# Performance work log

Hardware: AMD Instinct MI355X
Metric: run time of the kernel (lower is better)

Reference implementation:

```python
import jax, jax.numpy as jnp
import numpy as np

N_NODES = 50000
N_EDGES = 800000
NEG_SLOPE = 0.2  # PyG GATv2Conv default
EPS = 1e-16      # PyG softmax denominator epsilon


def _segment_softmax(logits, seg, num_segments):
    # logits: [E, H]; seg: [E] target-node ids
    m = jax.ops.segment_max(logits, seg, num_segments=num_segments)
    p = jnp.exp(logits - m[seg])
    s = jax.ops.segment_sum(p, seg, num_segments=num_segments)
    return p / (s[seg] + EPS)


def _gatv2_conv(x, src, dst, Wl, Wr, att, bias, heads, out_ch, concat):
    # x: [N, F]; Wl/Wr: [F, heads*out_ch]; att: [heads, out_ch]
    n = x.shape[0]
    xl = (x @ Wl).reshape(n, heads, out_ch)
    xr = (x @ Wr).reshape(n, heads, out_ch)
    # GATv2: e_ij = att . leaky_relu(xl[j] + xr[i]) for edge j->i
    e = jax.nn.leaky_relu(xl[src] + xr[dst], NEG_SLOPE)  # [E, H, C]
    logit = jnp.einsum('ehc,hc->eh', e, att)             # [E, H]
    alpha = _segment_softmax(logit, dst, n)              # [E, H]
    out = jax.ops.segment_sum(alpha[:, :, None] * xl[src], dst, num_segments=n)  # [N, H, C]
    if concat:
        out = out.reshape(n, heads * out_ch)
    else:
        out = out.mean(axis=1)
    return out + bias


def setup_inputs() -> dict:
    key = jax.random.key(0)
    ks = jax.random.split(key, 20)
    in_ch, hid, out_ch, heads, edge_dim = 128, 128, 64, 8, 6
    c1 = hid // heads  # 16
    g = lambda k, shp, fan: (jax.random.normal(k, shp, jnp.float32) / np.sqrt(fan)).astype(jnp.float32)
    inp = {
        'x': jax.random.normal(ks[0], (N_NODES, in_ch), jnp.float32),
        'edge_index': jax.random.randint(ks[1], (2, N_EDGES), 0, N_NODES, dtype=jnp.int64),
        'edge_attr': jax.random.normal(ks[2], (N_EDGES, edge_dim), jnp.float32),
        'Wl1': g(ks[3], (in_ch, heads * c1), in_ch),
        'Wr1': g(ks[4], (in_ch, heads * c1), in_ch),
        'att1': g(ks[5], (heads, c1), c1),
        'b1': jnp.zeros((heads * c1,), jnp.float32),
        # layer 2: GATv2Conv(hid -> out_ch, heads=1, no concat)
        'Wl2': g(ks[6], (hid, out_ch), hid),
        'Wr2': g(ks[7], (hid, out_ch), hid),
        'att2': g(ks[8], (1, out_ch), out_ch),
        'b2': jnp.zeros((out_ch,), jnp.float32),
        # edge encoder (computed but unused downstream, as in the source)
        'We1': g(ks[9], (edge_dim, hid), edge_dim), 'be1': jnp.zeros((hid,), jnp.float32),
        'We2': g(ks[10], (hid, hid), hid), 'be2': jnp.zeros((hid,), jnp.float32),
        # classifier
        'Wc1': g(ks[11], (out_ch, hid), out_ch), 'bc1': jnp.zeros((hid,), jnp.float32),
        'Wc2': g(ks[12], (hid, 2), hid), 'bc2': jnp.zeros((2,), jnp.float32),
    }
    return inp


def reference(x, edge_index, edge_attr, Wl1, Wr1, att1, b1, Wl2, Wr2, att2, b2,
              We1, be1, We2, be2, Wc1, bc1, Wc2, bc2):
    n = x.shape[0]
    # edge encoder (dead code in the original forward; kept for fidelity)
    _edge_feats = jax.nn.relu(edge_attr @ We1 + be1) @ We2 + be2
    # add self-loops (PyG GATv2Conv default add_self_loops=True)
    loop = jnp.arange(n, dtype=edge_index.dtype)
    src = jnp.concatenate([edge_index[0], loop])
    dst = jnp.concatenate([edge_index[1], loop])
    # layer 1 (heads=8, concat) + relu; dropout is identity in eval
    h = _gatv2_conv(x, src, dst, Wl1, Wr1, att1, b1, heads=8, out_ch=16, concat=True)
    h = jax.nn.relu(h)
    # layer 2 (heads=1, mean)
    emb = _gatv2_conv(h, src, dst, Wl2, Wr2, att2, b2, heads=1, out_ch=64, concat=False)
    logits = jax.nn.relu(emb @ Wc1 + bc1) @ Wc2 + bc2
    return emb, logits
```

## Files before the change

kernel.cpp:

```cpp
#include <hip/hip_runtime.h>
#include <hip/hip_bf16.h>
#include <cfloat>

#define N_NODES 50000
#define N_EDGES 800000
#define E_TOT   850000
#define NEG_SLOPE 0.2f
#define SM_EPS 1e-16f
#define SCAN_B 196
#define LOG2E 1.4426950408889634f

#define NCH 32
#define CSZ 25000
#define NR  8
#define RSZ 6250

typedef __attribute__((ext_vector_type(8))) short short8;
typedef __attribute__((ext_vector_type(4))) float f32x4;

__device__ __forceinline__ float lrelu(float v) { return v > 0.0f ? v : NEG_SLOPE * v; }

__device__ __forceinline__ unsigned f2bf_pack2(float a, float b) {
    unsigned ua = __float_as_uint(a);
    ua += 0x7fff + ((ua >> 16) & 1);
    unsigned ub = __float_as_uint(b);
    ub += 0x7fff + ((ub >> 16) & 1);
    return (ua >> 16) | (ub & 0xffff0000u);
}
__device__ __forceinline__ unsigned short f2bf(float a) {
    unsigned ua = __float_as_uint(a);
    ua += 0x7fff + ((ua >> 16) & 1);
    return (unsigned short)(ua >> 16);
}
__device__ __forceinline__ float bf_lo(unsigned u) { return __uint_as_float(u << 16); }
__device__ __forceinline__ float bf_hi(unsigned u) { return __uint_as_float(u & 0xffff0000u); }

__device__ __forceinline__ unsigned short pack_one(const float* __restrict__ B0,
                                                   const float* __restrict__ B1,
                                                   int i, int N) {
    int m   = i / (128 * N);
    int rem = i % (128 * N);
    int j    = rem & 7;
    int quad = (rem >> 3) & 3;
    int n    = (rem >> 5) & 15;
    int ctk  = rem >> 9;
    int ct   = ctk % (N / 16);
    int kt   = ctk / (N / 16);
    int k    = kt * 32 + quad * 8 + j;
    int col  = ct * 16 + n;
    const float* B = m ? B1 : B0;
    return f2bf(B[k * N + col]);
}

__global__ void prep(const float* __restrict__ Wl1, const float* __restrict__ Wr1,
                     const float* __restrict__ Wl2, const float* __restrict__ Wr2,
                     const float* __restrict__ Wc1,
                     unsigned short* __restrict__ Bp1, unsigned short* __restrict__ Bp2,
                     unsigned short* __restrict__ Wc1p,
                     int* __restrict__ flags) {
    int i = blockIdx.x * 256 + threadIdx.x;
    if (i < 32768) {
        Bp1[i] = pack_one(Wl1, Wr1, i, 128);
    } else if (i < 49152) {
        Bp2[i - 32768] = pack_one(Wl2, Wr2, i - 32768, 64);
    } else if (i < 57344) {
        int idx = i - 49152;
        int j    = idx & 7;
        int quad = (idx >> 3) & 3;
        int n    = (idx >> 5) & 15;
        int ctk  = idx >> 9;
        int ct   = ctk & 7;
        int kt   = ctk >> 3;
        Wc1p[idx] = f2bf(Wc1[(kt * 32 + quad * 8 + j) * 128 + ct * 16 + n]);
    } else if (i < 57600) {
        flags[i - 57344] = 0;
    }
}

__device__ __forceinline__ void gemm128_both(int b, const float* __restrict__ x,
                                             const unsigned short* __restrict__ Bp1,
                                             unsigned short* __restrict__ xlbf,
                                             float* __restrict__ xr1, int M) {
    int w = threadIdx.x >> 6, lane = threadIdx.x & 63;
    int quad = lane >> 4, l16 = lane & 15;
    int row0 = b * 32 + (w & 1) * 16;
    int cb   = (w >> 1) * 64;
    f32x4 accL[4], accR[4];
    #pragma unroll
    for (int t = 0; t < 4; ++t) {
        accL[t] = (f32x4){0.f, 0.f, 0.f, 0.f};
        accR[t] = (f32x4){0.f, 0.f, 0.f, 0.f};
    }
    int arow = row0 + l16;
    bool aok = arow < M;
    #pragma unroll
    for (int kt = 0; kt < 4; ++kt) {
        short8 a = (short8)0;
        if (aok) {
            const float* Ap = x + (size_t)arow * 128 + quad * 8 + kt * 32;
            float4 f0 = *(const float4*)(Ap);
            float4 f1 = *(const float4*)(Ap + 4);
            union { uint4 u; short8 s; } cv;
            cv.u.x = f2bf_pack2(f0.x, f0.y);
            cv.u.y = f2bf_pack2(f0.z, f0.w);
            cv.u.z = f2bf_pack2(f1.x, f1.y);
            cv.u.w = f2bf_pack2(f1.z, f1.w);
            a = cv.s;
        }
        #pragma unroll
        for (int t = 0; t < 4; ++t) {
            int ct = (cb >> 4) + t;
            const short* bp = (const short*)Bp1 + (((kt * 8 + ct) * 16 + l16) * 4 + quad) * 8;
            short8 bL = *(const short8*)bp;
            short8 bR = *(const short8*)(bp + 128 * 128);
            accL[t] = __builtin_amdgcn_mfma_f32_16x16x32_bf16(a, bL, accL[t], 0, 0, 0);
            accR[t] = __builtin_amdgcn_mfma_f32_16x16x32_bf16(a, bR, accR[t], 0, 0, 0);
        }
    }
    #pragma unroll
    for (int t = 0; t < 4; ++t) {
        int col = cb + t * 16 + l16;
        #pragma unroll
        for (int r = 0; r < 4; ++r) {
            int row = row0 + quad * 4 + r;
            if (row < M) {
                xlbf[(size_t)row * 128 + col] = f2bf(accL[t][r]);
                xr1[(size_t)row * 128 + col]  = accR[t][r];
            }
        }
    }
}

__global__ __launch_bounds__(256)
void k2_count_gemms(const int* __restrict__ ei, unsigned* __restrict__ hist,
                    unsigned short* __restrict__ rank16,
                    const float* __restrict__ x, const unsigned short* __restrict__ Bp1,
                    unsigned short* __restrict__ xlbf, float* __restrict__ xr1, int M) {
    __shared__ unsigned hcnt[RSZ];
    int b = blockIdx.x;
    if (b < NR * NCH) {
        int r = b >> 5, c = b & 31;
        for (int i = threadIdx.x; i < RSZ; i += 256) hcnt[i] = 0;
        int nz = __syncthreads_or(ei[2 * threadIdx.x + 1]);
        int nlo = r * RSZ, nhi = nlo + RSZ;
        int cbeg = c * CSZ, cend = cbeg + CSZ;
        for (int e = cbeg + (int)threadIdx.x; e < cend; e += 1024) {
            int dd[4];
            #pragma unroll
            for (int j = 0; j < 4; ++j) {
                int ee = e + j * 256;
                dd[j] = -1;
                if (ee < cend)
                    dd[j] = nz ? ei[N_EDGES + ee] : ei[2 * N_EDGES + 2 * ee];
            }
            #pragma unroll
            for (int j = 0; j < 4; ++j) {
                int d = dd[j];
                if (d >= nlo && d < nhi) {
                    unsigned rk = atomicAdd(&hcnt[d - nlo], 1u);
                    rank16[e + j * 256] = (unsigned short)rk;
                }
            }
        }
        __syncthreads();
        unsigned* hp = hist + (size_t)(r * NCH + c) * RSZ;
        for (int i = threadIdx.x; i < RSZ; i += 256) hp[i] = hcnt[i];
    } else {
        gemm128_both(b - NR * NCH, x, Bp1, xlbf, xr1, M);
    }
}

__global__ void scan_fused(const unsigned* __restrict__ hist, int* __restrict__ rowptr,
                           int* __restrict__ esrc, int* __restrict__ bsum,
                           int* __restrict__ flags, int* __restrict__ base) {
    __shared__ int sh[256];
    int b = blockIdx.x, t = threadIdx.x, i = b * 256 + t;
    unsigned d[NCH];
    int tot = 0;
    int rr = 0, q = 0;
    if (i < N_NODES) {
        rr = i / RSZ; q = i - rr * RSZ;
        const unsigned* hp = hist + (size_t)rr * NCH * RSZ + q;
        #pragma unroll
        for (int c = 0; c < NCH; ++c) { d[c] = hp[(size_t)c * RSZ]; tot += (int)d[c]; }
    }
    int v = (i < N_NODES) ? tot + 1 : 0;
    sh[t] = v;
    __syncthreads();
    int val = v;
    for (int off = 1; off < 256; off <<= 1) {
        int add = (t >= off) ? sh[t - off] : 0;
        __syncthreads();
        val += add; sh[t] = val;
        __syncthreads();
    }
    if (t == 255) {
        bsum[b] = val;
        __threadfence();
        atomicExch(&flags[b], 1);
    }
    int contrib = 0;
    if (t < b) {
        while (atomicAdd(&flags[t], 0) == 0) {}
        contrib = atomicAdd(&bsum[t], 0);
    }
    __syncthreads();
    sh[t] = contrib;
    __syncthreads();
    #pragma unroll
    for (int off = 128; off; off >>= 1) {
        if (t < off) sh[t] += sh[t + off];
        __syncthreads();
    }
    int offset = sh[0];
    if (i < N_NODES) {
        int rp = (val - v) + offset;
        rowptr[i] = rp;
        esrc[rp] = i;
        int acc = rp + 1;
        int* bp = base + (size_t)rr * NCH * RSZ + q;
        #pragma unroll
        for (int c = 0; c < NCH; ++c) { bp[(size_t)c * RSZ] = acc; acc += (int)d[c]; }
    }
    if (i == 0) rowptr[N_NODES] = E_TOT;
}

__global__ void scatter_edges(const int* __restrict__ ei, const int* __restrict__ base,
                              const unsigned short* __restrict__ rank16,
                              int* __restrict__ esrc) {
    int nz = __syncthreads_or(ei[2 * threadIdx.x + 1]);
    int i = blockIdx.x * blockDim.x + threadIdx.x;
    if (2 * i >= N_EDGES) return;
    bool has2 = (2 * i + 1 < N_EDGES);
    int s0, d0, s1 = 0, d1 = 0;
    if (nz) {
        int2 sp = *(const int2*)(ei + 2 * i);
        int2 dp = *(const int2*)(ei + N_EDGES + 2 * i);
        s0 = sp.x; s1 = sp.y; d0 = dp.x; d1 = dp.y;
    } else {
        int4 sp = *(const int4*)(ei + 4 * i);
        int4 dp = *(const int4*)(ei + 2 * N_EDGES + 4 * i);
        s0 = sp.x; s1 = sp.z; d0 = dp.x; d1 = dp.z;
    }
    unsigned rr = *(const unsigned*)(rank16 + 2 * i);
    int e0 = 2 * i, e1 = 2 * i + 1;
    int c0 = e0 / CSZ, c1 = e1 / CSZ;
    int r0 = d0 / RSZ, r1 = d1 / RSZ;
    esrc[base[((size_t)r0 * NCH + c0) * RSZ + (d0 - r0 * RSZ)] + (int)(rr & 0xffffu)] = s0;
    if (has2)
        esrc[base[((size_t)r1 * NCH + c1) * RSZ + (d1 - r1 * RSZ)] + (int)(rr >> 16)] = s1;
}

__global__ __launch_bounds__(256)
void gemm_mfma64(const unsigned short* __restrict__ Abf, const unsigned short* __restrict__ Bp,
                 unsigned short* __restrict__ C0bf, float* __restrict__ C1, int M) {
    int w = threadIdx.x >> 6, lane = threadIdx.x & 63;
    int quad = lane >> 4, l16 = lane & 15;
    int matrix = w >> 1;
    int row0 = blockIdx.x * 32 + (w & 1) * 16;
    const unsigned short* Bm = Bp + matrix * 128 * 64;
    f32x4 acc[4];
    #pragma unroll
    for (int t = 0; t < 4; ++t) acc[t] = (f32x4){0.f, 0.f, 0.f, 0.f};
    int arow = row0 + l16;
    bool aok = arow < M;
    const short* Ap = (const short*)Abf + (size_t)arow * 128 + quad * 8;
    #pragma unroll
    for (int kt = 0; kt < 4; ++kt) {
        short8 a = (short8)0;
        if (aok) a = *(const short8*)(Ap + kt * 32);
        #pragma unroll
        for (int t = 0; t < 4; ++t) {
            const short* bp = (const short*)Bm + (((kt * 4 + t) * 16 + l16) * 4 + quad) * 8;
            short8 bfr = *(const short8*)bp;
            acc[t] = __builtin_amdgcn_mfma_f32_16x16x32_bf16(a, bfr, acc[t], 0, 0, 0);
        }
    }
    #pragma unroll
    for (int t = 0; t < 4; ++t) {
        int col = t * 16 + l16;
        #pragma unroll
        for (int r = 0; r < 4; ++r) {
            int row = row0 + quad * 4 + r;
            if (row < M) {
                if (matrix) C1[(size_t)row * 64 + col] = acc[t][r];
                else        C0bf[(size_t)row * 64 + col] = f2bf(acc[t][r]);
            }
        }
    }
}

__global__ __launch_bounds__(256)
void node_fused1(const int* __restrict__ rowptr, const int* __restrict__ esrc,
                 const unsigned short* __restrict__ xlbf, const float* __restrict__ xr,
                 const float* __restrict__ att, const float* __restrict__ b1,
                 unsigned short* __restrict__ hbf) {
    int wave = threadIdx.x >> 6;
    int lane = threadIdx.x & 63;
    int n = blockIdx.x * 4 + wave;
    int slot = lane >> 4;
    int l = lane & 15;
    int beg = rowptr[n], end = rowptr[n + 1];
    const float* xrp = xr + (size_t)n * 128 + 8 * l;
    float4 xra = *(const float4*)(xrp);
    float4 xrb = *(const float4*)(xrp + 4);
    float4 ata = *(const float4*)(att + 8 * l);
    float4 atb = *(const float4*)(att + 8 * l + 4);
    const float c6 = 0.6f * LOG2E, c4 = 0.4f * LOG2E;
    float4 a6, a4, b6, b4c;
    a6.x = ata.x * c6; a6.y = ata.y * c6; a6.z = ata.z * c6; a6.w = ata.w * c6;
    a4.x = ata.x * c4; a4.y = ata.y * c4; a4.z = ata.z * c4; a4.w = ata.w * c4;
    b6.x = atb.x * c6; b6.y = atb.y * c6; b6.z = atb.z * c6; b6.w = atb.w * c6;
    b4c.x = atb.x * c4; b4c.y = atb.y * c4; b4c.z = atb.z * c4; b4c.w = atb.w * c4;
    float den = 0.0f;
    float4 aa = {0, 0, 0, 0}, ab = {0, 0, 0, 0};

    auto ldrow = [&](int s) -> uint4 {
        return *(const uint4*)(xlbf + (size_t)s * 128 + 8 * l);
    };
    int k0 = beg + slot;
    int sA = esrc[k0 < end ? k0 : beg];
    int sB = esrc[k0 + 4 < end ? k0 + 4 : beg];
    uint4 uA = ldrow(sA);

    for (int k = k0; k < end; k += 4) {
        uint4 uN = ldrow(sB);
        int sN = esrc[k + 8 < end ? k + 8 : beg];
        float x0 = bf_lo(uA.x), x1 = bf_hi(uA.x);
        float x2 = bf_lo(uA.y), x3 = bf_hi(uA.y);
        float x4 = bf_lo(uA.z), x5 = bf_hi(uA.z);
        float x6 = bf_lo(uA.w), x7 = bf_hi(uA.w);
        float t0 = x0 + xra.x, t1 = x1 + xra.y, t2 = x2 + xra.z, t3 = x3 + xra.w;
        float t4 = x4 + xrb.x, t5 = x5 + xrb.y, t6 = x6 + xrb.z, t7 = x7 + xrb.w;
        float v = 0.0f;
        v = __builtin_fmaf(a6.x, t0, v); v = __builtin_fmaf(a4.x, __builtin_fabsf(t0), v);
        v = __builtin_fmaf(a6.y, t1, v); v = __builtin_fmaf(a4.y, __builtin_fabsf(t1), v);
        v = __builtin_fmaf(a6.z, t2, v); v = __builtin_fmaf(a4.z, __builtin_fabsf(t2), v);
        v = __builtin_fmaf(a6.w, t3, v); v = __builtin_fmaf(a4.w, __builtin_fabsf(t3), v);
        v = __builtin_fmaf(b6.x, t4, v); v = __builtin_fmaf(b4c.x, __builtin_fabsf(t4), v);
        v = __builtin_fmaf(b6.y, t5, v); v = __builtin_fmaf(b4c.y, __builtin_fabsf(t5), v);
        v = __builtin_fmaf(b6.z, t6, v); v = __builtin_fmaf(b4c.z, __builtin_fabsf(t6), v);
        v = __builtin_fmaf(b6.w, t7, v); v = __builtin_fmaf(b4c.w, __builtin_fabsf(t7), v);
        v += __shfl_xor(v, 1);
        float p = exp2f(v);
        den += p;
        aa.x = __builtin_fmaf(p, x0, aa.x); aa.y = __builtin_fmaf(p, x1, aa.y);
        aa.z = __builtin_fmaf(p, x2, aa.z); aa.w = __builtin_fmaf(p, x3, aa.w);
        ab.x = __builtin_fmaf(p, x4, ab.x); ab.y = __builtin_fmaf(p, x5, ab.y);
        ab.z = __builtin_fmaf(p, x6, ab.z); ab.w = __builtin_fmaf(p, x7, ab.w);
        uA = uN; sB = sN;
    }

    #pragma unroll
    for (int off = 16; off < 64; off <<= 1) {
        aa.x += __shfl_xor(aa.x, off); aa.y += __shfl_xor(aa.y, off);
        aa.z += __shfl_xor(aa.z, off); aa.w += __shfl_xor(aa.w, off);
        ab.x += __shfl_xor(ab.x, off); ab.y += __shfl_xor(ab.y, off);
        ab.z += __shfl_xor(ab.z, off); ab.w += __shfl_xor(ab.w, off);
        den   += __shfl_xor(den, off);
    }
    if (slot == 0) {
        float inv = 1.0f / (den + SM_EPS);
        float4 b4a = *(const float4*)(b1 + 8 * l);
        float4 b4b = *(const float4*)(b1 + 8 * l + 4);
        float oa0 = fmaxf(aa.x * inv + b4a.x, 0.0f);
        float oa1 = fmaxf(aa.y * inv + b4a.y, 0.0f);
        float oa2 = fmaxf(aa.z * inv + b4a.z, 0.0f);
        float oa3 = fmaxf(aa.w * inv + b4a.w, 0.0f);
        float ob0 = fmaxf(ab.x * inv + b4b.x, 0.0f);
        float ob1 = fmaxf(ab.y * inv + b4b.y, 0.0f);
        float ob2 = fmaxf(ab.z * inv + b4b.z, 0.0f);
        float ob3 = fmaxf(ab.w * inv + b4b.w, 0.0f);
        uint4 pk;
        pk.x = f2bf_pack2(oa0, oa1);
        pk.y = f2bf_pack2(oa2, oa3);
        pk.z = f2bf_pack2(ob0, ob1);
        pk.w = f2bf_pack2(ob2, ob3);
        *(uint4*)(hbf + (size_t)n * 128 + 8 * l) = pk;
    }
}

__global__ __launch_bounds__(256)
void node_fused2(const int* __restrict__ rowptr, const int* __restrict__ esrc,
                 const unsigned short* __restrict__ xlbf, const float* __restrict__ xr,
                 const float* __restrict__ att, const float* __restrict__ b2v,
                 float* __restrict__ out_emb, unsigned short* __restrict__ embbf) {
    int wave = threadIdx.x >> 6;
    int lane = threadIdx.x & 63;
    int n = blockIdx.x * 4 + wave;
    int slot = lane >> 3;
    int l = lane & 7;
    int beg = rowptr[n], end = rowptr[n + 1];
    const float* xrp = xr + (size_t)n * 64 + 8 * l;
    float4 xra = *(const float4*)(xrp);
    float4 xrb = *(const float4*)(xrp + 4);
    float4 ata = *(const float4*)(att + 8 * l);
    float4 atb = *(const float4*)(att + 8 * l + 4);
    const float c6 = 0.6f * LOG2E, c4 = 0.4f * LOG2E;
    float4 a6, a4, b6, b4c;
    a6.x = ata.x * c6; a6.y = ata.y * c6; a6.z = ata.z * c6; a6.w = ata.w * c6;
    a4.x = ata.x * c4; a4.y = ata.y * c4; a4.z = ata.z * c4; a4.w = ata.w * c4;
    b6.x = atb.x * c6; b6.y = atb.y * c6; b6.z = atb.z * c6; b6.w = atb.w * c6;
    b4c.x = atb.x * c4; b4c.y = atb.y * c4; b4c.z = atb.z * c4; b4c.w = atb.w * c4;
    float den = 0.0f;
    float4 aa = {0, 0, 0, 0}, ab = {0, 0, 0, 0};

    auto ldrow = [&](int s) -> uint4 {
        return *(const uint4*)(xlbf + (size_t)s * 64 + 8 * l);
    };
    int k0 = beg + slot;
    int sA = esrc[k0 < end ? k0 : beg];
    int sB = esrc[k0 + 8 < end ? k0 + 8 : beg];
    uint4 uA = ldrow(sA);

    for (int k = k0; k < end; k += 8) {
        uint4 uN = ldrow(sB);
        int sN = esrc[k + 16 < end ? k + 16 : beg];
        float x0 = bf_lo(uA.x), x1 = bf_hi(uA.x);
        float x2 = bf_lo(uA.y), x3 = bf_hi(uA.y);
        float x4 = bf_lo(uA.z), x5 = bf_hi(uA.z);
        float x6 = bf_lo(uA.w), x7 = bf_hi(uA.w);
        float t0 = x0 + xra.x, t1 = x1 + xra.y, t2 = x2 + xra.z, t3 = x3 + xra.w;
        float t4 = x4 + xrb.x, t5 = x5 + xrb.y, t6 = x6 + xrb.z, t7 = x7 + xrb.w;
        float v = 0.0f;
        v = __builtin_fmaf(a6.x, t0, v); v = __builtin_fmaf(a4.x, __builtin_fabsf(t0), v);
        v = __builtin_fmaf(a6.y, t1, v); v = __builtin_fmaf(a4.y, __builtin_fabsf(t1), v);
        v = __builtin_fmaf(a6.z, t2, v); v = __builtin_fmaf(a4.z, __builtin_fabsf(t2), v);
        v = __builtin_fmaf(a6.w, t3, v); v = __builtin_fmaf(a4.w, __builtin_fabsf(t3), v);
        v = __builtin_fmaf(b6.x, t4, v); v = __builtin_fmaf(b4c.x, __builtin_fabsf(t4), v);
        v = __builtin_fmaf(b6.y, t5, v); v = __builtin_fmaf(b4c.y, __builtin_fabsf(t5), v);
        v = __builtin_fmaf(b6.z, t6, v); v = __builtin_fmaf(b4c.z, __builtin_fabsf(t6), v);
        v = __builtin_fmaf(b6.w, t7, v); v = __builtin_fmaf(b4c.w, __builtin_fabsf(t7), v);
        v += __shfl_xor(v, 1);
        v += __shfl_xor(v, 2);
        v += __shfl_xor(v, 4);
        float p = exp2f(v);
        den += p;
        aa.x = __builtin_fmaf(p, x0, aa.x); aa.y = __builtin_fmaf(p, x1, aa.y);
        aa.z = __builtin_fmaf(p, x2, aa.z); aa.w = __builtin_fmaf(p, x3, aa.w);
        ab.x = __builtin_fmaf(p, x4, ab.x); ab.y = __builtin_fmaf(p, x5, ab.y);
        ab.z = __builtin_fmaf(p, x6, ab.z); ab.w = __builtin_fmaf(p, x7, ab.w);
        uA = uN; sB = sN;
    }

    #pragma unroll
    for (int off = 8; off < 64; off <<= 1) {
        aa.x += __shfl_xor(aa.x, off); aa.y += __shfl_xor(aa.y, off);
        aa.z += __shfl_xor(aa.z, off); aa.w += __shfl_xor(aa.w, off);
        ab.x += __shfl_xor(ab.x, off); ab.y += __shfl_xor(ab.y, off);
        ab.z += __shfl_xor(ab.z, off); ab.w += __shfl_xor(ab.w, off);
        den   += __shfl_xor(den, off);
    }
    if (slot == 0) {
        float inv = 1.0f / (den + SM_EPS);
        float4 b4a = *(const float4*)(b2v + 8 * l);
        float4 b4b = *(const float4*)(b2v + 8 * l + 4);
        float4 ea, eb;
        ea.x = aa.x * inv + b4a.x; ea.y = aa.y * inv + b4a.y;
        ea.z = aa.z * inv + b4a.z; ea.w = aa.w * inv + b4a.w;
        eb.x = ab.x * inv + b4b.x; eb.y = ab.y * inv + b4b.y;
        eb.z = ab.z * inv + b4b.z; eb.w = ab.w * inv + b4b.w;
        float* op = out_emb + (size_t)n * 64 + 8 * l;
        *(float4*)(op)     = ea;
        *(float4*)(op + 4) = eb;
        uint4 pk;
        pk.x = f2bf_pack2(ea.x, ea.y);
        pk.y = f2bf_pack2(ea.z, ea.w);
        pk.z = f2bf_pack2(eb.x, eb.y);
        pk.w = f2bf_pack2(eb.z, eb.w);
        *(uint4*)(embbf + (size_t)n * 64 + 8 * l) = pk;
    }
}

__global__ __launch_bounds__(256)
void cls_mfma(const unsigned short* __restrict__ embbf, const unsigned short* __restrict__ Wc1p,
              const float* __restrict__ bc1, const float* __restrict__ Wc2,
              const float* __restrict__ bc2, float* __restrict__ out_logits) {
    __shared__ float part[2][16][2][2];
    int w = threadIdx.x >> 6, lane = threadIdx.x & 63;
    int quad = lane >> 4, l16 = lane & 15;
    int rowhalf = w & 1, colhalf = w >> 1;
    int row0 = blockIdx.x * 32 + rowhalf * 16;
    int cb = colhalf * 64;
    f32x4 acc[4];
    #pragma unroll
    for (int t = 0; t < 4; ++t) acc[t] = (f32x4){0.f, 0.f, 0.f, 0.f};
    int arow = row0 + l16;
    bool aok = arow < N_NODES;
    const short* Ap = (const short*)embbf + (size_t)arow * 64 + quad * 8;
    #pragma unroll
    for (int kt = 0; kt < 2; ++kt) {
        short8 a = (short8)0;
        if (aok) a = *(const short8*)(Ap + kt * 32);
        #pragma unroll
        for (int t = 0; t < 4; ++t) {
            int ct = colhalf * 4 + t;
            const short* bp = (const short*)Wc1p + (((kt * 8 + ct) * 16 + l16) * 4 + quad) * 8;
            short8 bfr = *(const short8*)bp;
            acc[t] = __builtin_amdgcn_mfma_f32_16x16x32_bf16(a, bfr, acc[t], 0, 0, 0);
        }
    }
    float p0[4] = {0, 0, 0, 0}, p1[4] = {0, 0, 0, 0};
    #pragma unroll
    for (int t = 0; t < 4; ++t) {
        int col = cb + t * 16 + l16;
        float w2a = Wc2[2 * col], w2b = Wc2[2 * col + 1];
        float bc = bc1[col];
        #pragma unroll
        for (int r = 0; r < 4; ++r) {
            float tv = fmaxf(acc[t][r] + bc, 0.0f);
            p0[r] += tv * w2a;
            p1[r] += tv * w2b;
        }
    }
    #pragma unroll
    for (int off = 1; off < 16; off <<= 1) {
        #pragma unroll
        for (int r = 0; r < 4; ++r) {
            p0[r] += __shfl_xor(p0[r], off);
            p1[r] += __shfl_xor(p1[r], off);
        }
    }
    if (l16 == 0) {
        #pragma unroll
        for (int r = 0; r < 4; ++r) {
            part[rowhalf][quad * 4 + r][colhalf][0] = p0[r];
            part[rowhalf][quad * 4 + r][colhalf][1] = p1[r];
        }
    }
    __syncthreads();
    int t = threadIdx.x;
    if (t < 64) {
        int row = t >> 1, c = t & 1;
        int rh = row >> 4, r16 = row & 15;
        float s = part[rh][r16][0][c] + part[rh][r16][1][c] + bc2[c];
        int n = blockIdx.x * 32 + row;
        if (n < N_NODES) out_logits[(size_t)n * 2 + c] = s;
    }
}

extern "C" void kernel_launch(void* const* d_in, const int* in_sizes, int n_in,
                              void* d_out, int out_size, void* d_ws, size_t ws_size,
                              hipStream_t stream) {
    const float* x    = (const float*)d_in[0];
    const int*   ei   = (const int*)d_in[1];
    const float* Wl1  = (const float*)d_in[3];
    const float* Wr1  = (const float*)d_in[4];
    const float* att1 = (const float*)d_in[5];
    const float* b1   = (const float*)d_in[6];
    const float* Wl2  = (const float*)d_in[7];
    const float* Wr2  = (const float*)d_in[8];
    const float* att2 = (const float*)d_in[9];
    const float* b2   = (const float*)d_in[10];
    const float* Wc1  = (const float*)d_in[15];
    const float* bc1  = (const float*)d_in[16];
    const float* Wc2  = (const float*)d_in[17];
    const float* bc2  = (const float*)d_in[18];

    float* ws = (float*)d_ws;
    int* rowptr = (int*)ws + 50000;
    int* esrc   = rowptr + 50016;
    int* bsum   = esrc + 850000;
    int* flags  = bsum + 256;
    unsigned short* rank16 = (unsigned short*)(flags + 256);
    float* xr1           = ws + 1400448;
    unsigned short* xlbf = (unsigned short*)(ws + 7800448);
    unsigned short* hbf  = (unsigned short*)(ws + 11000448);
    unsigned* hist = (unsigned*)(ws + 11000448);
    int* base      = (int*)(ws + 12600448);
    unsigned short* Bp1   = (unsigned short*)(ws + 14200448);
    unsigned short* Bp2   = (unsigned short*)(ws + 14216832);
    unsigned short* Wc1p  = (unsigned short*)(ws + 14225024);
    unsigned short* embbf = (unsigned short*)(ws + 14229120);

    float* out_emb    = (float*)d_out;
    float* out_logits = out_emb + (size_t)N_NODES * 64;

    prep<<<225, 256, 0, stream>>>(Wl1, Wr1, Wl2, Wr2, Wc1, Bp1, Bp2, Wc1p, flags);

    k2_count_gemms<<<256 + 1563, 256, 0, stream>>>(ei, hist, rank16, x, Bp1, xlbf, xr1, N_NODES);

    scan_fused<<<SCAN_B, 256, 0, stream>>>(hist, rowptr, esrc, bsum, flags, base);

    scatter_edges<<<1563, 256, 0, stream>>>(ei, base, rank16, esrc);

    node_fused1<<<12500, 256, 0, stream>>>(rowptr, esrc, xlbf, xr1, att1, b1, hbf);

    gemm_mfma64<<<1563, 256, 0, stream>>>(hbf, Bp2, xlbf, xr1, N_NODES);
    node_fused2<<<12500, 256, 0, stream>>>(rowptr, esrc, xlbf, xr1, att2, b2, out_emb, embbf);

    cls_mfma<<<1563, 256, 0, stream>>>(embbf, Wc1p, bc1, Wc2, bc2, out_logits);
}
```

Before: 273.9 us.

## Split layer-1 aggregation into two channel-half passes with packed float2 math

The layer-1 aggregation kernel now handles 64 of the 128 channels per launch and runs twice. Each wave uses 8 lanes per edge and 8 edge slots instead of 16 lanes and 4 slots. The per-pass gather working set is half of each xl row, which is meant to improve cache locality. More edges are in flight per wave, and packed f32x2 FMAs are used for the logit and accumulation math. The cost is reading esrc, rowptr and xr twice and paying for one extra kernel launch.

```diff
diff --git a/kernel.cpp b/kernel.cpp
--- a/kernel.cpp
+++ b/kernel.cpp
@@ -17,6 +17,7 @@
 
 typedef __attribute__((ext_vector_type(8))) short short8;
 typedef __attribute__((ext_vector_type(4))) float f32x4;
+typedef __attribute__((ext_vector_type(2))) float f32x2;
 
 __device__ __forceinline__ float lrelu(float v) { return v > 0.0f ? v : NEG_SLOPE * v; }
 
@@ -34,6 +35,18 @@
 }
 __device__ __forceinline__ float bf_lo(unsigned u) { return __uint_as_float(u << 16); }
 __device__ __forceinline__ float bf_hi(unsigned u) { return __uint_as_float(u & 0xffff0000u); }
+__device__ __forceinline__ f32x2 bf_unpk(unsigned u) {
+    f32x2 r;
+    r.x = __uint_as_float(u << 16);
+    r.y = __uint_as_float(u & 0xffff0000u);
+    return r;
+}
+__device__ __forceinline__ f32x2 fabs2(f32x2 a) {
+    f32x2 r;
+    r.x = __uint_as_float(__float_as_uint(a.x) & 0x7fffffffu);
+    r.y = __uint_as_float(__float_as_uint(a.y) & 0x7fffffffu);
+    return r;
+}
 
 __device__ __forceinline__ unsigned short pack_one(const float* __restrict__ B0,
                                                    const float* __restrict__ B1,
@@ -291,92 +304,90 @@
 }
 
 __global__ __launch_bounds__(256)
-void node_fused1(const int* __restrict__ rowptr, const int* __restrict__ esrc,
-                 const unsigned short* __restrict__ xlbf, const float* __restrict__ xr,
-                 const float* __restrict__ att, const float* __restrict__ b1,
-                 unsigned short* __restrict__ hbf) {
+void node_fused1h(const int* __restrict__ rowptr, const int* __restrict__ esrc,
+                  const unsigned short* __restrict__ xlbf, const float* __restrict__ xr,
+                  const float* __restrict__ att, const float* __restrict__ b1,
+                  unsigned short* __restrict__ hbf, int ch_off) {
     int wave = threadIdx.x >> 6;
     int lane = threadIdx.x & 63;
     int n = blockIdx.x * 4 + wave;
-    int slot = lane >> 4;
-    int l = lane & 15;
+    int slot = lane >> 3;
+    int l = lane & 7;
+    int ch = ch_off + 8 * l;
     int beg = rowptr[n], end = rowptr[n + 1];
-    const float* xrp = xr + (size_t)n * 128 + 8 * l;
-    float4 xra = *(const float4*)(xrp);
-    float4 xrb = *(const float4*)(xrp + 4);
-    float4 ata = *(const float4*)(att + 8 * l);
-    float4 atb = *(const float4*)(att + 8 * l + 4);
+    const float* xrp = xr + (size_t)n * 128 + ch;
+    f32x2 xrv[4];
+    #pragma unroll
+    for (int j = 0; j < 4; ++j) xrv[j] = *(const f32x2*)(xrp + 2 * j);
+    const float* atp = att + ch;
     const float c6 = 0.6f * LOG2E, c4 = 0.4f * LOG2E;
-    float4 a6, a4, b6, b4c;
-    a6.x = ata.x * c6; a6.y = ata.y * c6; a6.z = ata.z * c6; a6.w = ata.w * c6;
-    a4.x = ata.x * c4; a4.y = ata.y * c4; a4.z = ata.z * c4; a4.w = ata.w * c4;
-    b6.x = atb.x * c6; b6.y = atb.y * c6; b6.z = atb.z * c6; b6.w = atb.w * c6;
-    b4c.x = atb.x * c4; b4c.y = atb.y * c4; b4c.z = atb.z * c4; b4c.w = atb.w * c4;
+    f32x2 a6[4], a4[4];
+    #pragma unroll
+    for (int j = 0; j < 4; ++j) {
+        f32x2 a = *(const f32x2*)(atp + 2 * j);
+        a6[j] = a * c6;
+        a4[j] = a * c4;
+    }
     float den = 0.0f;
-    float4 aa = {0, 0, 0, 0}, ab = {0, 0, 0, 0};
+    f32x2 acc[4];
+    #pragma unroll
+    for (int j = 0; j < 4; ++j) acc[j] = (f32x2){0.f, 0.f};
 
     auto ldrow = [&](int s) -> uint4 {
-        return *(const uint4*)(xlbf + (size_t)s * 128 + 8 * l);
+        return *(const uint4*)(xlbf + (size_t)s * 128 + ch);
     };
     int k0 = beg + slot;
     int sA = esrc[k0 < end ? k0 : beg];
-    int sB = esrc[k0 + 4 < end ? k0 + 4 : beg];
+    int sB = esrc[k0 + 8 < end ? k0 + 8 : beg];
     uint4 uA = ldrow(sA);
 
-    for (int k = k0; k < end; k += 4) {
+    for (int k = k0; k < end; k += 8) {
         uint4 uN = ldrow(sB);
-        int sN = esrc[k + 8 < end ? k + 8 : beg];
-        float x0 = bf_lo(uA.x), x1 = bf_hi(uA.x);
-        float x2 = bf_lo(uA.y), x3 = bf_hi(uA.y);
-        float x4 = bf_lo(uA.z), x5 = bf_hi(uA.z);
-        float x6 = bf_lo(uA.w), x7 = bf_hi(uA.w);
-        float t0 = x0 + xra.x, t1 = x1 + xra.y, t2 = x2 + xra.z, t3 = x3 + xra.w;
-        float t4 = x4 + xrb.x, t5 = x5 + xrb.y, t6 = x6 + xrb.z, t7 = x7 + xrb.w;
-        float v = 0.0f;
-        v = __builtin_fmaf(a6.x, t0, v); v = __builtin_fmaf(a4.x, __builtin_fabsf(t0), v);
-        v = __builtin_fmaf(a6.y, t1, v); v = __builtin_fmaf(a4.y, __builtin_fabsf(t1), v);
-        v = __builtin_fmaf(a6.z, t2, v); v = __builtin_fmaf(a4.z, __builtin_fabsf(t2), v);
-        v = __builtin_fmaf(a6.w, t3, v); v = __builtin_fmaf(a4.w, __builtin_fabsf(t3), v);
-        v = __builtin_fmaf(b6.x, t4, v); v = __builtin_fmaf(b4c.x, __builtin_fabsf(t4), v);
-        v = __builtin_fmaf(b6.y, t5, v); v = __builtin_fmaf(b4c.y, __builtin_fabsf(t5), v);
-        v = __builtin_fmaf(b6.z, t6, v); v = __builtin_fmaf(b4c.z, __builtin_fabsf(t6), v);
-        v = __builtin_fmaf(b6.w, t7, v); v = __builtin_fmaf(b4c.w, __builtin_fabsf(t7), v);
+        int sN = esrc[k + 16 < end ? k + 16 : beg];
+        unsigned uu[4] = {uA.x, uA.y, uA.z, uA.w};
+        f32x2 xv[4];
+        f32x2 v2 = {0.f, 0.f};
+        #pragma unroll
+        for (int j = 0; j < 4; ++j) {
+            xv[j] = bf_unpk(uu[j]);
+            f32x2 t = xv[j] + xrv[j];
+            v2 = __builtin_elementwise_fma(a6[j], t, v2);
+            v2 = __builtin_elementwise_fma(a4[j], fabs2(t), v2);
+        }
+        float v = v2.x + v2.y;
         v += __shfl_xor(v, 1);
         float p = exp2f(v);
         den += p;
-        aa.x = __builtin_fmaf(p, x0, aa.x); aa.y = __builtin_fmaf(p, x1, aa.y);
-        aa.z = __builtin_fmaf(p, x2, aa.z); aa.w = __builtin_fmaf(p, x3, aa.w);
-        ab.x = __builtin_fmaf(p, x4, ab.x); ab.y = __builtin_fmaf(p, x5, ab.y);
-        ab.z = __builtin_fmaf(p, x6, ab.z); ab.w = __builtin_fmaf(p, x7, ab.w);
+        f32x2 p2 = {p, p};
+        #pragma unroll
+        for (int j = 0; j < 4; ++j) acc[j] = __builtin_elementwise_fma(p2, xv[j], acc[j]);
         uA = uN; sB = sN;
     }
 
     #pragma unroll
-    for (int off = 16; off < 64; off <<= 1) {
-        aa.x += __shfl_xor(aa.x, off); aa.y += __shfl_xor(aa.y, off);
-        aa.z += __shfl_xor(aa.z, off); aa.w += __shfl_xor(aa.w, off);
-        ab.x += __shfl_xor(ab.x, off); ab.y += __shfl_xor(ab.y, off);
-        ab.z += __shfl_xor(ab.z, off); ab.w += __shfl_xor(ab.w, off);
-        den   += __shfl_xor(den, off);
+    for (int off = 8; off < 64; off <<= 1) {
+        #pragma unroll
+        for (int j = 0; j < 4; ++j) {
+            acc[j].x += __shfl_xor(acc[j].x, off);
+            acc[j].y += __shfl_xor(acc[j].y, off);
+        }
+        den += __shfl_xor(den, off);
     }
     if (slot == 0) {
         float inv = 1.0f / (den + SM_EPS);
-        float4 b4a = *(const float4*)(b1 + 8 * l);
-        float4 b4b = *(const float4*)(b1 + 8 * l + 4);
-        float oa0 = fmaxf(aa.x * inv + b4a.x, 0.0f);
-        float oa1 = fmaxf(aa.y * inv + b4a.y, 0.0f);
-        float oa2 = fmaxf(aa.z * inv + b4a.z, 0.0f);
-        float oa3 = fmaxf(aa.w * inv + b4a.w, 0.0f);
-        float ob0 = fmaxf(ab.x * inv + b4b.x, 0.0f);
-        float ob1 = fmaxf(ab.y * inv + b4b.y, 0.0f);
-        float ob2 = fmaxf(ab.z * inv + b4b.z, 0.0f);
-        float ob3 = fmaxf(ab.w * inv + b4b.w, 0.0f);
+        const float* bp = b1 + ch;
+        float o[8];
+        #pragma unroll
+        for (int j = 0; j < 4; ++j) {
+            o[2 * j]     = fmaxf(__builtin_fmaf(acc[j].x, inv, bp[2 * j]), 0.0f);
+            o[2 * j + 1] = fmaxf(__builtin_fmaf(acc[j].y, inv, bp[2 * j + 1]), 0.0f);
+        }
         uint4 pk;
-        pk.x = f2bf_pack2(oa0, oa1);
-        pk.y = f2bf_pack2(oa2, oa3);
-        pk.z = f2bf_pack2(ob0, ob1);
-        pk.w = f2bf_pack2(ob2, ob3);
-        *(uint4*)(hbf + (size_t)n * 128 + 8 * l) = pk;
+        pk.x = f2bf_pack2(o[0], o[1]);
+        pk.y = f2bf_pack2(o[2], o[3]);
+        pk.z = f2bf_pack2(o[4], o[5]);
+        pk.w = f2bf_pack2(o[6], o[7]);
+        *(uint4*)(hbf + (size_t)n * 128 + ch) = pk;
     }
 }
 
@@ -584,7 +595,8 @@
 
     scatter_edges<<<1563, 256, 0, stream>>>(ei, base, rank16, esrc);
 
-    node_fused1<<<12500, 256, 0, stream>>>(rowptr, esrc, xlbf, xr1, att1, b1, hbf);
+    node_fused1h<<<12500, 256, 0, stream>>>(rowptr, esrc, xlbf, xr1, att1, b1, hbf, 0);
+    node_fused1h<<<12500, 256, 0, stream>>>(rowptr, esrc, xlbf, xr1, att1, b1, hbf, 64);
 
     gemm_mfma64<<<1563, 256, 0, stream>>>(hbf, Bp2, xlbf, xr1, N_NODES);
     node_fused2<<<12500, 256, 0, stream>>>(rowptr, esrc, xlbf, xr1, att2, b2, out_emb, embbf);
```

New measurement: 302.8 us. +10.6%, slower.
